# Optimization experiments

Measured on AMD Instinct MI355X. Metric: run time of the kernel, lower is better.

## Reference

```python
import jax, jax.numpy as jnp
import numpy as np

N_NODES = 200_000
N_EDGES = 6_400_000
N_GRAPHS = 512


def _sage_conv(x, edge_index, Wl, bl, Wr):
    """PyG SAGEConv (mean aggr): lin_l(mean_j x_j) + lin_r(x_i).
    lin_l has bias, lin_r does not. Messages flow src -> dst."""
    src, dst = edge_index[0], edge_index[1]
    n = x.shape[0]
    # gather neighbor features [E, F] and segment-mean into dst nodes
    msg_sum = jax.ops.segment_sum(x[src], dst, num_segments=n)
    deg = jax.ops.segment_sum(jnp.ones((src.shape[0],), x.dtype), dst, num_segments=n)
    mean = msg_sum / jnp.maximum(deg, 1.0)[:, None]  # zero in-degree -> 0
    return mean @ Wl.T + bl + x @ Wr.T


def setup_inputs() -> dict:
    key = jax.random.key(0)
    ks = jax.random.split(key, 9)
    x = jax.random.normal(ks[0], (N_NODES, 1), dtype=jnp.float32)
    edge_index = jax.random.randint(ks[1], (2, N_EDGES), 0, N_NODES, dtype=jnp.int64)
    batch = jnp.sort(jax.random.randint(ks[2], (N_NODES,), 0, N_GRAPHS, dtype=jnp.int64))
    W1l = jax.random.normal(ks[3], (16, 1), dtype=jnp.float32)
    b1 = jax.random.normal(ks[4], (16,), dtype=jnp.float32)
    W1r = jax.random.normal(ks[5], (16, 1), dtype=jnp.float32)
    W2l = jax.random.normal(ks[6], (1, 16), dtype=jnp.float32)
    b2 = jax.random.normal(ks[7], (1,), dtype=jnp.float32)
    W2r = jax.random.normal(ks[8], (1, 16), dtype=jnp.float32)
    return {"x": x, "edge_index": edge_index, "batch": batch, "batch_size": N_GRAPHS,
            "W1l": W1l, "b1": b1, "W1r": W1r, "W2l": W2l, "b2": b2, "W2r": W2r}


def reference(x, edge_index, batch, batch_size, W1l, b1, W1r, W2l, b2, W2r):
    h = _sage_conv(x, edge_index, W1l, b1, W1r)          # [N, 16]
    h = jax.nn.relu(h)
    h = _sage_conv(h, edge_index, W2l, b2, W2r)          # [N, 1]
    # global_add_pool: segment-sum node features by graph id
    out = jax.ops.segment_sum(h, batch, num_segments=batch_size)  # [B, 1]
    return out
```

## Files before the change

kernel.cpp:

```cpp
#include <hip/hip_runtime.h>


#define PP        16
#define BLK       1024
#define SCAP      1024u
#define SMASK     1023u
#define TILE      (BLK * 4)
#define CBIN      32
#define CNT_ONE   (1u << 25)
#define FX_BIAS   131072
#define SCALE     4096.0f
#define INV_SCALE (1.0f / 4096.0f)

__global__ __launch_bounds__(BLK) void partition_kernel(
    const int* __restrict__ ei, unsigned* __restrict__ pairs,
    unsigned* __restrict__ tails, int E, int bins, unsigned Mdiv, int cap) {
    extern __shared__ unsigned buf[];
    __shared__ unsigned cnt[PP], base[PP], fq[PP], gb[PP];
    const int tid = threadIdx.x;
    if (tid < PP) { cnt[tid] = 0; base[tid] = 0; }
    __syncthreads();

    int b0 = blockIdx.x * TILE;
    int e0 = b0 + tid * 4;
    int nv = E - e0; nv = nv < 0 ? 0 : (nv > 4 ? 4 : nv);
    int srcv[4], dstv[4];
    if (nv == 4 && ((E & 3) == 0)) {
        int4 s = *(const int4*)(ei + e0);
        int4 d = *(const int4*)(ei + E + e0);
        srcv[0] = s.x; srcv[1] = s.y; srcv[2] = s.z; srcv[3] = s.w;
        dstv[0] = d.x; dstv[1] = d.y; dstv[2] = d.z; dstv[3] = d.w;
    } else {
        for (int j = 0; j < nv; ++j) { srcv[j] = ei[e0 + j]; dstv[j] = ei[E + e0 + j]; }
    }
    unsigned w[4]; int part[4]; bool pend[4];
    for (int j = 0; j < 4; ++j) {
        pend[j] = (j < nv);
        if (pend[j]) {
            unsigned dst = (unsigned)dstv[j];
            unsigned pt = (unsigned)(((unsigned long long)dst * Mdiv) >> 32);
            int ld = (int)dst - (int)pt * bins;
            while (ld >= bins) { ld -= bins; ++pt; }
            while (ld < 0)     { ld += bins; --pt; }
            part[j] = (int)pt;
            w[j] = ((unsigned)srcv[j] << 14) | (unsigned)ld;
        }
    }
    for (int j = 0; j < 4; ++j) {
        if (pend[j]) {
            unsigned slot = atomicAdd(&cnt[part[j]], 1u);
            if (slot - base[part[j]] < SCAP) {
                buf[part[j] * SCAP + (slot & SMASK)] = w[j]; pend[j] = false;
            } else atomicSub(&cnt[part[j]], 1u);
        }
    }
    int npend = __syncthreads_count((int)(pend[0] | pend[1] | pend[2] | pend[3]));
    while (npend > 0) {
        if (tid < PP) {
            unsigned avail = cnt[tid] - base[tid];
            unsigned f = avail & ~511u;
            fq[tid] = f;
            if (f) gb[tid] = atomicAdd(&tails[tid], f);
        }
        __syncthreads();
        {
            int wv = tid >> 6, lane = tid & 63;
            unsigned f = fq[wv];
            if (f) {
                unsigned g0 = gb[wv], bs = base[wv];
                unsigned mx = (g0 + f <= (unsigned)cap) ? f : ((unsigned)cap > g0 ? (unsigned)cap - g0 : 0u);
                unsigned* dp = pairs + (size_t)wv * cap + g0;
                for (unsigned jj = lane; jj < mx; jj += 64)
                    dp[jj] = buf[wv * SCAP + ((bs + jj) & SMASK)];
            }
        }
        __syncthreads();
        if (tid < PP) base[tid] += fq[tid];
        __syncthreads();
        for (int j = 0; j < 4; ++j) {
            if (pend[j]) {
                unsigned slot = atomicAdd(&cnt[part[j]], 1u);
                if (slot - base[part[j]] < SCAP) {
                    buf[part[j] * SCAP + (slot & SMASK)] = w[j]; pend[j] = false;
                } else atomicSub(&cnt[part[j]], 1u);
            }
        }
        npend = __syncthreads_count((int)(pend[0] | pend[1] | pend[2] | pend[3]));
    }
    if (tid < PP) {
        unsigned avail = cnt[tid] - base[tid];
        fq[tid] = avail;
        if (avail) gb[tid] = atomicAdd(&tails[tid], avail);
    }
    __syncthreads();
    {
        int wv = tid >> 6, lane = tid & 63;
        unsigned f = fq[wv];
        if (f) {
            unsigned g0 = gb[wv], bs = base[wv];
            unsigned mx = (g0 + f <= (unsigned)cap) ? f : ((unsigned)cap > g0 ? (unsigned)cap - g0 : 0u);
            unsigned* dp = pairs + (size_t)wv * cap + g0;
            for (unsigned jj = lane; jj < mx; jj += 64)
                dp[jj] = buf[wv * SCAP + ((bs + jj) & SMASK)];
        }
    }
}

__global__ __launch_bounds__(BLK, 8) void bin1_kernel(
    const unsigned* __restrict__ pairs, const unsigned* __restrict__ tails,
    const float* __restrict__ x, unsigned* __restrict__ slab,
    int N, int bins, int cap) {
    extern __shared__ unsigned sb[];
    int p = blockIdx.x & (PP - 1);
    int c = blockIdx.x / PP;
    int len = (int)tails[p]; if (len > cap) len = cap;
    int st = (int)((long long)len * c / CBIN);
    int en = (int)((long long)len * (c + 1) / CBIN);
    for (int j = threadIdx.x; j < bins; j += BLK) sb[j] = 0;
    __syncthreads();
    const unsigned* bp = pairs + (size_t)p * cap;
    int st4 = (st + 3) & ~3;
    int en4 = en & ~3;
    int preEnd = st4 < en ? st4 : en;
    for (int e = st + (int)threadIdx.x; e < preEnd; e += BLK) {
        unsigned wv = bp[e];
        atomicAdd(&sb[wv & 16383u],
                  CNT_ONE + (unsigned)((int)rintf(x[wv >> 14] * SCALE) + FX_BIAS));
    }
    if (st4 < en4) {
        const uint4* bp4 = (const uint4*)(bp + st4);
        int n4 = (en4 - st4) >> 2;
        for (int e = threadIdx.x; e < n4; e += BLK) {
            uint4 wq = bp4[e];
            atomicAdd(&sb[wq.x & 16383u],
                      CNT_ONE + (unsigned)((int)rintf(x[wq.x >> 14] * SCALE) + FX_BIAS));
            atomicAdd(&sb[wq.y & 16383u],
                      CNT_ONE + (unsigned)((int)rintf(x[wq.y >> 14] * SCALE) + FX_BIAS));
            atomicAdd(&sb[wq.z & 16383u],
                      CNT_ONE + (unsigned)((int)rintf(x[wq.z >> 14] * SCALE) + FX_BIAS));
            atomicAdd(&sb[wq.w & 16383u],
                      CNT_ONE + (unsigned)((int)rintf(x[wq.w >> 14] * SCALE) + FX_BIAS));
        }
    }
    int tailSt = st4 > en4 ? st4 : en4;
    for (int e = tailSt + (int)threadIdx.x; e < en; e += BLK) {
        unsigned wv = bp[e];
        atomicAdd(&sb[wv & 16383u],
                  CNT_ONE + (unsigned)((int)rintf(x[wv >> 14] * SCALE) + FX_BIAS));
    }
    __syncthreads();
    unsigned* dst = slab + (size_t)c * N + (size_t)p * bins;
    int nb = N - p * bins; if (nb > bins) nb = bins;
    for (int j = threadIdx.x; j < nb; j += BLK) dst[j] = sb[j];
}

__global__ __launch_bounds__(BLK, 8) void bin2_kernel(
    const unsigned* __restrict__ pairs, const unsigned* __restrict__ tails,
    const float* __restrict__ pv, int* __restrict__ slab,
    int N, int bins, int cap) {
    extern __shared__ int sbi[];
    int p = blockIdx.x & (PP - 1);
    int c = blockIdx.x / PP;
    int len = (int)tails[p]; if (len > cap) len = cap;
    int st = (int)((long long)len * c / CBIN);
    int en = (int)((long long)len * (c + 1) / CBIN);
    for (int j = threadIdx.x; j < bins; j += BLK) sbi[j] = 0;
    __syncthreads();
    const unsigned* bp = pairs + (size_t)p * cap;
    int st4 = (st + 3) & ~3;
    int en4 = en & ~3;
    int preEnd = st4 < en ? st4 : en;
    for (int e = st + (int)threadIdx.x; e < preEnd; e += BLK) {
        unsigned wv = bp[e];
        atomicAdd(&sbi[wv & 16383u], (int)rintf(pv[wv >> 14] * SCALE));
    }
    if (st4 < en4) {
        const uint4* bp4 = (const uint4*)(bp + st4);
        int n4 = (en4 - st4) >> 2;
        for (int e = threadIdx.x; e < n4; e += BLK) {
            uint4 wq = bp4[e];
            atomicAdd(&sbi[wq.x & 16383u], (int)rintf(pv[wq.x >> 14] * SCALE));
            atomicAdd(&sbi[wq.y & 16383u], (int)rintf(pv[wq.y >> 14] * SCALE));
            atomicAdd(&sbi[wq.z & 16383u], (int)rintf(pv[wq.z >> 14] * SCALE));
            atomicAdd(&sbi[wq.w & 16383u], (int)rintf(pv[wq.w >> 14] * SCALE));
        }
    }
    int tailSt = st4 > en4 ? st4 : en4;
    for (int e = tailSt + (int)threadIdx.x; e < en; e += BLK) {
        unsigned wv = bp[e];
        atomicAdd(&sbi[wv & 16383u], (int)rintf(pv[wv >> 14] * SCALE));
    }
    __syncthreads();
    int* dst = slab + (size_t)c * N + (size_t)p * bins;
    int nb = N - p * bins; if (nb > bins) nb = bins;
    for (int j = threadIdx.x; j < nb; j += BLK) dst[j] = sbi[j];
}

__global__ void node_pass1_kernel(const float* __restrict__ x,
                                  const unsigned* __restrict__ slab,
                                  const float* __restrict__ W1l,
                                  const float* __restrict__ b1,
                                  const float* __restrict__ W1r,
                                  const float* __restrict__ W2l,
                                  const float* __restrict__ W2r,
                                  float* __restrict__ deg_out,
                                  float* __restrict__ pv,
                                  float* __restrict__ qv,
                                  int N) {
    __shared__ float s_w1l[16], s_b1[16], s_w1r[16], s_w2l[16], s_w2r[16];
    if (threadIdx.x < 16) {
        s_w1l[threadIdx.x] = W1l[threadIdx.x];
        s_b1[threadIdx.x]  = b1[threadIdx.x];
        s_w1r[threadIdx.x] = W1r[threadIdx.x];
        s_w2l[threadIdx.x] = W2l[threadIdx.x];
        s_w2r[threadIdx.x] = W2r[threadIdx.x];
    }
    __syncthreads();
    int n = blockIdx.x * blockDim.x + threadIdx.x;
    if (n >= N) return;

    unsigned cnt = 0, fx = 0;
#pragma unroll
    for (int c = 0; c < CBIN; ++c) {
        unsigned w = slab[(size_t)c * N + n];
        cnt += w >> 25;
        fx  += w & (CNT_ONE - 1);
    }
    float dg  = (float)cnt;
    float sum = (float)(int)(fx - cnt * (unsigned)FX_BIAS) * INV_SCALE;
    float m   = sum / fmaxf(dg, 1.0f);

    float xv = x[n];
    float pa = 0.0f, qa = 0.0f;
#pragma unroll
    for (int f = 0; f < 16; ++f) {
        float h = fmaf(m, s_w1l[f], fmaf(xv, s_w1r[f], s_b1[f]));
        h = fmaxf(h, 0.0f);
        pa = fmaf(h, s_w2l[f], pa);
        qa = fmaf(h, s_w2r[f], qa);
    }
    deg_out[n] = dg;
    pv[n] = pa;
    qv[n] = qa;
}

__global__ void node_pass2_kernel(const int* __restrict__ slab2,
                                  const float* __restrict__ deg,
                                  const float* __restrict__ qv,
                                  const float* __restrict__ b2,
                                  const int* __restrict__ batch,
                                  float* __restrict__ out,
                                  int N) {
    int i = blockIdx.x * blockDim.x + threadIdx.x;
    float b2v = b2[0];
    float val = 0.0f;
    int g;
    if (i < N) {
        int sacc = 0;
#pragma unroll
        for (int c = 0; c < CBIN; ++c) sacc += slab2[(size_t)c * N + i];
        float s2 = (float)sacc * INV_SCALE;
        val = s2 / fmaxf(deg[i], 1.0f) + b2v + qv[i];
        g = batch[i];
    } else {
        g = batch[N - 1];
    }
    int g0 = __shfl(g, 0);
    unsigned long long same = __ballot(g == g0);
    if (same == ~0ULL) {
        for (int off = 32; off > 0; off >>= 1) val += __shfl_down(val, off);
        if ((threadIdx.x & 63) == 0) atomicAdd(&out[g0], val);
    } else {
        atomicAdd(&out[g], val);
    }
}

extern "C" void kernel_launch(void* const* d_in, const int* in_sizes, int n_in,
                              void* d_out, int out_size, void* d_ws, size_t ws_size,
                              hipStream_t stream) {
    const float* x     = (const float*)d_in[0];
    const int*   ei    = (const int*)d_in[1];
    const int*   batch = (const int*)d_in[2];
    const float* W1l = (const float*)d_in[4];
    const float* b1  = (const float*)d_in[5];
    const float* W1r = (const float*)d_in[6];
    const float* W2l = (const float*)d_in[7];
    const float* b2  = (const float*)d_in[8];
    const float* W2r = (const float*)d_in[9];

    const int N = in_sizes[0];
    const int E = in_sizes[1] / 2;
    float* out = (float*)d_out;

    const int bins = (N + PP - 1) / PP;
    const unsigned Mdiv =
        (unsigned)(((1ULL << 32) + (unsigned)bins - 1) / (unsigned)bins);
    const int EperP = E / PP;
    int cap = ((EperP + EperP / 32 + 4096) + 1023) & ~1023;

    unsigned* pairs = (unsigned*)d_ws;
    unsigned* slab1 = pairs + (size_t)PP * cap;
    int*      slab2 = (int*)slab1;
    float* deg = (float*)(slab1 + (size_t)CBIN * N);
    float* pv  = deg + N;
    float* qv  = pv + N;
    unsigned* tails = (unsigned*)(qv + N);

    hipMemsetAsync(d_out, 0, (size_t)out_size * sizeof(float), stream);
    hipMemsetAsync(tails, 0, PP * sizeof(unsigned), stream);

    const int partShmem = PP * (int)SCAP * 4;
    const int binShmem  = bins * 4;
    hipFuncSetAttribute((const void*)partition_kernel,
                        hipFuncAttributeMaxDynamicSharedMemorySize, partShmem);
    hipFuncSetAttribute((const void*)bin1_kernel,
                        hipFuncAttributeMaxDynamicSharedMemorySize, binShmem);
    hipFuncSetAttribute((const void*)bin2_kernel,
                        hipFuncAttributeMaxDynamicSharedMemorySize, binShmem);

    int partBlocks = (E + TILE - 1) / TILE;
    const int NB = 256;
    int node_blocks = (N + NB - 1) / NB;

    partition_kernel<<<partBlocks, BLK, partShmem, stream>>>(ei, pairs, tails,
                                                             E, bins, Mdiv, cap);
    bin1_kernel<<<PP * CBIN, BLK, binShmem, stream>>>(pairs, tails, x, slab1,
                                                      N, bins, cap);
    node_pass1_kernel<<<node_blocks, NB, 0, stream>>>(x, slab1, W1l, b1, W1r,
                                                      W2l, W2r, deg, pv, qv, N);
    bin2_kernel<<<PP * CBIN, BLK, binShmem, stream>>>(pairs, tails, pv, slab2,
                                                      N, bins, cap);
    node_pass2_kernel<<<node_blocks, NB, 0, stream>>>(slab2, deg, qv, b2, batch,
                                                      out, N);
}
```

Measured before the change: 228.0 us.

## Replace partition-and-bin aggregation with direct global atomic scatter per edge

Removes the shared-memory partitioning pass and the LDS-binned slab reductions. Each edge pass now reads edge indices directly and performs global atomicAdd into per-node packed fixed-point accumulators, zeroed by a memset. This eliminates the intermediate pairs buffer write/read and the 32-way slab reduction, at the cost of 6.4M random global atomics per pass with no locality.

```diff
diff --git a/kernel.cpp b/kernel.cpp
--- a/kernel.cpp
+++ b/kernel.cpp
@@ -1,203 +1,62 @@
 #include <hip/hip_runtime.h>
 
 
-#define PP        16
-#define BLK       1024
-#define SCAP      1024u
-#define SMASK     1023u
-#define TILE      (BLK * 4)
-#define CBIN      32
 #define CNT_ONE   (1u << 25)
 #define FX_BIAS   131072
 #define SCALE     4096.0f
 #define INV_SCALE (1.0f / 4096.0f)
 
-__global__ __launch_bounds__(BLK) void partition_kernel(
-    const int* __restrict__ ei, unsigned* __restrict__ pairs,
-    unsigned* __restrict__ tails, int E, int bins, unsigned Mdiv, int cap) {
-    extern __shared__ unsigned buf[];
-    __shared__ unsigned cnt[PP], base[PP], fq[PP], gb[PP];
-    const int tid = threadIdx.x;
-    if (tid < PP) { cnt[tid] = 0; base[tid] = 0; }
-    __syncthreads();
-
-    int b0 = blockIdx.x * TILE;
-    int e0 = b0 + tid * 4;
-    int nv = E - e0; nv = nv < 0 ? 0 : (nv > 4 ? 4 : nv);
-    int srcv[4], dstv[4];
-    if (nv == 4 && ((E & 3) == 0)) {
+__global__ __launch_bounds__(256) void edge1_kernel(
+    const int* __restrict__ ei, const float* __restrict__ x,
+    unsigned* __restrict__ acc1, int E) {
+    int t = blockIdx.x * blockDim.x + threadIdx.x;
+    int e0 = t * 4;
+    if (e0 + 4 <= E) {
         int4 s = *(const int4*)(ei + e0);
         int4 d = *(const int4*)(ei + E + e0);
-        srcv[0] = s.x; srcv[1] = s.y; srcv[2] = s.z; srcv[3] = s.w;
-        dstv[0] = d.x; dstv[1] = d.y; dstv[2] = d.z; dstv[3] = d.w;
+        unsigned w0 = CNT_ONE + (unsigned)((int)rintf(x[s.x] * SCALE) + FX_BIAS);
+        unsigned w1 = CNT_ONE + (unsigned)((int)rintf(x[s.y] * SCALE) + FX_BIAS);
+        unsigned w2 = CNT_ONE + (unsigned)((int)rintf(x[s.z] * SCALE) + FX_BIAS);
+        unsigned w3 = CNT_ONE + (unsigned)((int)rintf(x[s.w] * SCALE) + FX_BIAS);
+        atomicAdd(&acc1[d.x], w0);
+        atomicAdd(&acc1[d.y], w1);
+        atomicAdd(&acc1[d.z], w2);
+        atomicAdd(&acc1[d.w], w3);
     } else {
-        for (int j = 0; j < nv; ++j) { srcv[j] = ei[e0 + j]; dstv[j] = ei[E + e0 + j]; }
-    }
-    unsigned w[4]; int part[4]; bool pend[4];
-    for (int j = 0; j < 4; ++j) {
-        pend[j] = (j < nv);
-        if (pend[j]) {
-            unsigned dst = (unsigned)dstv[j];
-            unsigned pt = (unsigned)(((unsigned long long)dst * Mdiv) >> 32);
-            int ld = (int)dst - (int)pt * bins;
-            while (ld >= bins) { ld -= bins; ++pt; }
-            while (ld < 0)     { ld += bins; --pt; }
-            part[j] = (int)pt;
-            w[j] = ((unsigned)srcv[j] << 14) | (unsigned)ld;
-        }
-    }
-    for (int j = 0; j < 4; ++j) {
-        if (pend[j]) {
-            unsigned slot = atomicAdd(&cnt[part[j]], 1u);
-            if (slot - base[part[j]] < SCAP) {
-                buf[part[j] * SCAP + (slot & SMASK)] = w[j]; pend[j] = false;
-            } else atomicSub(&cnt[part[j]], 1u);
-        }
-    }
-    int npend = __syncthreads_count((int)(pend[0] | pend[1] | pend[2] | pend[3]));
-    while (npend > 0) {
-        if (tid < PP) {
-            unsigned avail = cnt[tid] - base[tid];
-            unsigned f = avail & ~511u;
-            fq[tid] = f;
-            if (f) gb[tid] = atomicAdd(&tails[tid], f);
-        }
-        __syncthreads();
-        {
-            int wv = tid >> 6, lane = tid & 63;
-            unsigned f = fq[wv];
-            if (f) {
-                unsigned g0 = gb[wv], bs = base[wv];
-                unsigned mx = (g0 + f <= (unsigned)cap) ? f : ((unsigned)cap > g0 ? (unsigned)cap - g0 : 0u);
-                unsigned* dp = pairs + (size_t)wv * cap + g0;
-                for (unsigned jj = lane; jj < mx; jj += 64)
-                    dp[jj] = buf[wv * SCAP + ((bs + jj) & SMASK)];
-            }
-        }
-        __syncthreads();
-        if (tid < PP) base[tid] += fq[tid];
-        __syncthreads();
-        for (int j = 0; j < 4; ++j) {
-            if (pend[j]) {
-                unsigned slot = atomicAdd(&cnt[part[j]], 1u);
-                if (slot - base[part[j]] < SCAP) {
-                    buf[part[j] * SCAP + (slot & SMASK)] = w[j]; pend[j] = false;
-                } else atomicSub(&cnt[part[j]], 1u);
-            }
-        }
-        npend = __syncthreads_count((int)(pend[0] | pend[1] | pend[2] | pend[3]));
-    }
-    if (tid < PP) {
-        unsigned avail = cnt[tid] - base[tid];
-        fq[tid] = avail;
-        if (avail) gb[tid] = atomicAdd(&tails[tid], avail);
-    }
-    __syncthreads();
-    {
-        int wv = tid >> 6, lane = tid & 63;
-        unsigned f = fq[wv];
-        if (f) {
-            unsigned g0 = gb[wv], bs = base[wv];
-            unsigned mx = (g0 + f <= (unsigned)cap) ? f : ((unsigned)cap > g0 ? (unsigned)cap - g0 : 0u);
-            unsigned* dp = pairs + (size_t)wv * cap + g0;
-            for (unsigned jj = lane; jj < mx; jj += 64)
-                dp[jj] = buf[wv * SCAP + ((bs + jj) & SMASK)];
+        for (int e = e0; e < E; ++e) {
+            int s = ei[e], d = ei[E + e];
+            atomicAdd(&acc1[d],
+                      CNT_ONE + (unsigned)((int)rintf(x[s] * SCALE) + FX_BIAS));
         }
     }
 }
 
-__global__ __launch_bounds__(BLK, 8) void bin1_kernel(
-    const unsigned* __restrict__ pairs, const unsigned* __restrict__ tails,
-    const float* __restrict__ x, unsigned* __restrict__ slab,
-    int N, int bins, int cap) {
-    extern __shared__ unsigned sb[];
-    int p = blockIdx.x & (PP - 1);
-    int c = blockIdx.x / PP;
-    int len = (int)tails[p]; if (len > cap) len = cap;
-    int st = (int)((long long)len * c / CBIN);
-    int en = (int)((long long)len * (c + 1) / CBIN);
-    for (int j = threadIdx.x; j < bins; j += BLK) sb[j] = 0;
-    __syncthreads();
-    const unsigned* bp = pairs + (size_t)p * cap;
-    int st4 = (st + 3) & ~3;
-    int en4 = en & ~3;
-    int preEnd = st4 < en ? st4 : en;
-    for (int e = st + (int)threadIdx.x; e < preEnd; e += BLK) {
-        unsigned wv = bp[e];
-        atomicAdd(&sb[wv & 16383u],
-                  CNT_ONE + (unsigned)((int)rintf(x[wv >> 14] * SCALE) + FX_BIAS));
-    }
-    if (st4 < en4) {
-        const uint4* bp4 = (const uint4*)(bp + st4);
-        int n4 = (en4 - st4) >> 2;
-        for (int e = threadIdx.x; e < n4; e += BLK) {
-            uint4 wq = bp4[e];
-            atomicAdd(&sb[wq.x & 16383u],
-                      CNT_ONE + (unsigned)((int)rintf(x[wq.x >> 14] * SCALE) + FX_BIAS));
-            atomicAdd(&sb[wq.y & 16383u],
-                      CNT_ONE + (unsigned)((int)rintf(x[wq.y >> 14] * SCALE) + FX_BIAS));
-            atomicAdd(&sb[wq.z & 16383u],
-                      CNT_ONE + (unsigned)((int)rintf(x[wq.z >> 14] * SCALE) + FX_BIAS));
-            atomicAdd(&sb[wq.w & 16383u],
-                      CNT_ONE + (unsigned)((int)rintf(x[wq.w >> 14] * SCALE) + FX_BIAS));
+__global__ __launch_bounds__(256) void edge2_kernel(
+    const int* __restrict__ ei, const float* __restrict__ pv,
+    int* __restrict__ acc2, int E) {
+    int t = blockIdx.x * blockDim.x + threadIdx.x;
+    int e0 = t * 4;
+    if (e0 + 4 <= E) {
+        int4 s = *(const int4*)(ei + e0);
+        int4 d = *(const int4*)(ei + E + e0);
+        int v0 = (int)rintf(pv[s.x] * SCALE);
+        int v1 = (int)rintf(pv[s.y] * SCALE);
+        int v2 = (int)rintf(pv[s.z] * SCALE);
+        int v3 = (int)rintf(pv[s.w] * SCALE);
+        atomicAdd(&acc2[d.x], v0);
+        atomicAdd(&acc2[d.y], v1);
+        atomicAdd(&acc2[d.z], v2);
+        atomicAdd(&acc2[d.w], v3);
+    } else {
+        for (int e = e0; e < E; ++e) {
+            int s = ei[e], d = ei[E + e];
+            atomicAdd(&acc2[d], (int)rintf(pv[s] * SCALE));
         }
     }
-    int tailSt = st4 > en4 ? st4 : en4;
-    for (int e = tailSt + (int)threadIdx.x; e < en; e += BLK) {
-        unsigned wv = bp[e];
-        atomicAdd(&sb[wv & 16383u],
-                  CNT_ONE + (unsigned)((int)rintf(x[wv >> 14] * SCALE) + FX_BIAS));
-    }
-    __syncthreads();
-    unsigned* dst = slab + (size_t)c * N + (size_t)p * bins;
-    int nb = N - p * bins; if (nb > bins) nb = bins;
-    for (int j = threadIdx.x; j < nb; j += BLK) dst[j] = sb[j];
-}
-
-__global__ __launch_bounds__(BLK, 8) void bin2_kernel(
-    const unsigned* __restrict__ pairs, const unsigned* __restrict__ tails,
-    const float* __restrict__ pv, int* __restrict__ slab,
-    int N, int bins, int cap) {
-    extern __shared__ int sbi[];
-    int p = blockIdx.x & (PP - 1);
-    int c = blockIdx.x / PP;
-    int len = (int)tails[p]; if (len > cap) len = cap;
-    int st = (int)((long long)len * c / CBIN);
-    int en = (int)((long long)len * (c + 1) / CBIN);
-    for (int j = threadIdx.x; j < bins; j += BLK) sbi[j] = 0;
-    __syncthreads();
-    const unsigned* bp = pairs + (size_t)p * cap;
-    int st4 = (st + 3) & ~3;
-    int en4 = en & ~3;
-    int preEnd = st4 < en ? st4 : en;
-    for (int e = st + (int)threadIdx.x; e < preEnd; e += BLK) {
-        unsigned wv = bp[e];
-        atomicAdd(&sbi[wv & 16383u], (int)rintf(pv[wv >> 14] * SCALE));
-    }
-    if (st4 < en4) {
-        const uint4* bp4 = (const uint4*)(bp + st4);
-        int n4 = (en4 - st4) >> 2;
-        for (int e = threadIdx.x; e < n4; e += BLK) {
-            uint4 wq = bp4[e];
-            atomicAdd(&sbi[wq.x & 16383u], (int)rintf(pv[wq.x >> 14] * SCALE));
-            atomicAdd(&sbi[wq.y & 16383u], (int)rintf(pv[wq.y >> 14] * SCALE));
-            atomicAdd(&sbi[wq.z & 16383u], (int)rintf(pv[wq.z >> 14] * SCALE));
-            atomicAdd(&sbi[wq.w & 16383u], (int)rintf(pv[wq.w >> 14] * SCALE));
-        }
-    }
-    int tailSt = st4 > en4 ? st4 : en4;
-    for (int e = tailSt + (int)threadIdx.x; e < en; e += BLK) {
-        unsigned wv = bp[e];
-        atomicAdd(&sbi[wv & 16383u], (int)rintf(pv[wv >> 14] * SCALE));
-    }
-    __syncthreads();
-    int* dst = slab + (size_t)c * N + (size_t)p * bins;
-    int nb = N - p * bins; if (nb > bins) nb = bins;
-    for (int j = threadIdx.x; j < nb; j += BLK) dst[j] = sbi[j];
 }
 
 __global__ void node_pass1_kernel(const float* __restrict__ x,
-                                  const unsigned* __restrict__ slab,
+                                  const unsigned* __restrict__ acc1,
                                   const float* __restrict__ W1l,
                                   const float* __restrict__ b1,
                                   const float* __restrict__ W1r,
@@ -219,13 +78,9 @@
     int n = blockIdx.x * blockDim.x + threadIdx.x;
     if (n >= N) return;
 
-    unsigned cnt = 0, fx = 0;
-#pragma unroll
-    for (int c = 0; c < CBIN; ++c) {
-        unsigned w = slab[(size_t)c * N + n];
-        cnt += w >> 25;
-        fx  += w & (CNT_ONE - 1);
-    }
+    unsigned w = acc1[n];
+    unsigned cnt = w >> 25;
+    unsigned fx  = w & (CNT_ONE - 1);
     float dg  = (float)cnt;
     float sum = (float)(int)(fx - cnt * (unsigned)FX_BIAS) * INV_SCALE;
     float m   = sum / fmaxf(dg, 1.0f);
@@ -244,7 +99,7 @@
     qv[n] = qa;
 }
 
-__global__ void node_pass2_kernel(const int* __restrict__ slab2,
+__global__ void node_pass2_kernel(const int* __restrict__ acc2,
                                   const float* __restrict__ deg,
                                   const float* __restrict__ qv,
                                   const float* __restrict__ b2,
@@ -256,10 +111,7 @@
     float val = 0.0f;
     int g;
     if (i < N) {
-        int sacc = 0;
-#pragma unroll
-        for (int c = 0; c < CBIN; ++c) sacc += slab2[(size_t)c * N + i];
-        float s2 = (float)sacc * INV_SCALE;
+        float s2 = (float)acc2[i] * INV_SCALE;
         val = s2 / fmaxf(deg[i], 1.0f) + b2v + qv[i];
         g = batch[i];
     } else {
@@ -292,44 +144,24 @@
     const int E = in_sizes[1] / 2;
     float* out = (float*)d_out;
 
-    const int bins = (N + PP - 1) / PP;
-    const unsigned Mdiv =
-        (unsigned)(((1ULL << 32) + (unsigned)bins - 1) / (unsigned)bins);
-    const int EperP = E / PP;
-    int cap = ((EperP + EperP / 32 + 4096) + 1023) & ~1023;
-
-    unsigned* pairs = (unsigned*)d_ws;
-    unsigned* slab1 = pairs + (size_t)PP * cap;
-    int*      slab2 = (int*)slab1;
-    float* deg = (float*)(slab1 + (size_t)CBIN * N);
+    unsigned* acc1 = (unsigned*)d_ws;
+    int*      acc2 = (int*)(acc1 + N);
+    float* deg = (float*)(acc2 + N);
     float* pv  = deg + N;
     float* qv  = pv + N;
-    unsigned* tails = (unsigned*)(qv + N);
 
     hipMemsetAsync(d_out, 0, (size_t)out_size * sizeof(float), stream);
-    hipMemsetAsync(tails, 0, PP * sizeof(unsigned), stream);
+    hipMemsetAsync(acc1, 0, (size_t)(2 * N) * 4, stream);
 
-    const int partShmem = PP * (int)SCAP * 4;
-    const int binShmem  = bins * 4;
-    hipFuncSetAttribute((const void*)partition_kernel,
-                        hipFuncAttributeMaxDynamicSharedMemorySize, partShmem);
-    hipFuncSetAttribute((const void*)bin1_kernel,
-                        hipFuncAttributeMaxDynamicSharedMemorySize, binShmem);
-    hipFuncSetAttribute((const void*)bin2_kernel,
-                        hipFuncAttributeMaxDynamicSharedMemorySize, binShmem);
-
-    int partBlocks = (E + TILE - 1) / TILE;
+    const int EB = 256;
+    int edge_blocks = (E / 4 + EB - 1) / EB;
     const int NB = 256;
     int node_blocks = (N + NB - 1) / NB;
 
-    partition_kernel<<<partBlocks, BLK, partShmem, stream>>>(ei, pairs, tails,
-                                                             E, bins, Mdiv, cap);
-    bin1_kernel<<<PP * CBIN, BLK, binShmem, stream>>>(pairs, tails, x, slab1,
-                                                      N, bins, cap);
-    node_pass1_kernel<<<node_blocks, NB, 0, stream>>>(x, slab1, W1l, b1, W1r,
+    edge1_kernel<<<edge_blocks, EB, 0, stream>>>(ei, x, acc1, E);
+    node_pass1_kernel<<<node_blocks, NB, 0, stream>>>(x, acc1, W1l, b1, W1r,
                                                       W2l, W2r, deg, pv, qv, N);
-    bin2_kernel<<<PP * CBIN, BLK, binShmem, stream>>>(pairs, tails, pv, slab2,
-                                                      N, bins, cap);
-    node_pass2_kernel<<<node_blocks, NB, 0, stream>>>(slab2, deg, qv, b2, batch,
+    edge2_kernel<<<edge_blocks, EB, 0, stream>>>(ei, pv, acc2, E);
+    node_pass2_kernel<<<node_blocks, NB, 0, stream>>>(acc2, deg, qv, b2, batch,
                                                       out, N);
 }
```

After: 622.0 us. 2.73x slower.

## Use power-of-two bins, prequantize gathers, and atomically merge partial histograms

Applied to the files above, without the earlier changes.

Partitions destinations with a 16384-node shift/mask instead of a magic-number division, which gives 13 partitions for this N instead of 16. Node features are quantized once up front, in a new prequant kernel and in node_pass1, so the per-edge loops only gather integers. Each bin block now atomically adds its nonzero LDS histogram entries into one global accumulator instead of writing a full per-chunk slab that the node kernels then reduce over 32 rows. This cuts slab traffic and reduction work, in exchange for global atomics, an extra launch, a larger memset, and a changed chunk count of 39.

```diff
diff --git a/kernel.cpp b/kernel.cpp
--- a/kernel.cpp
+++ b/kernel.cpp
@@ -1,24 +1,33 @@
 #include <hip/hip_runtime.h>
 
 
-#define PP        16
 #define BLK       1024
 #define SCAP      1024u
 #define SMASK     1023u
 #define TILE      (BLK * 4)
-#define CBIN      32
+#define BSH       14
+#define BINS      16384
+#define BMSK      16383u
+#define CBIN      39
 #define CNT_ONE   (1u << 25)
 #define FX_BIAS   131072
 #define SCALE     4096.0f
 #define INV_SCALE (1.0f / 4096.0f)
 
+__global__ __launch_bounds__(256) void prequant_kernel(
+    const float* __restrict__ x, unsigned* __restrict__ xq1, int N) {
+    int n = blockIdx.x * blockDim.x + threadIdx.x;
+    if (n < N)
+        xq1[n] = CNT_ONE + (unsigned)((int)rintf(x[n] * SCALE) + FX_BIAS);
+}
+
 __global__ __launch_bounds__(BLK) void partition_kernel(
     const int* __restrict__ ei, unsigned* __restrict__ pairs,
-    unsigned* __restrict__ tails, int E, int bins, unsigned Mdiv, int cap) {
+    unsigned* __restrict__ tails, int E, int cap, int pp) {
     extern __shared__ unsigned buf[];
-    __shared__ unsigned cnt[PP], base[PP], fq[PP], gb[PP];
+    __shared__ unsigned cnt[16], base[16], fq[16], gb[16];
     const int tid = threadIdx.x;
-    if (tid < PP) { cnt[tid] = 0; base[tid] = 0; }
+    if (tid < pp) { cnt[tid] = 0; base[tid] = 0; }
     __syncthreads();
 
     int b0 = blockIdx.x * TILE;
@@ -38,12 +47,8 @@
         pend[j] = (j < nv);
         if (pend[j]) {
             unsigned dst = (unsigned)dstv[j];
-            unsigned pt = (unsigned)(((unsigned long long)dst * Mdiv) >> 32);
-            int ld = (int)dst - (int)pt * bins;
-            while (ld >= bins) { ld -= bins; ++pt; }
-            while (ld < 0)     { ld += bins; --pt; }
-            part[j] = (int)pt;
-            w[j] = ((unsigned)srcv[j] << 14) | (unsigned)ld;
+            part[j] = (int)(dst >> BSH);
+            w[j] = ((unsigned)srcv[j] << BSH) | (dst & BMSK);
         }
     }
     for (int j = 0; j < 4; ++j) {
@@ -56,7 +61,7 @@
     }
     int npend = __syncthreads_count((int)(pend[0] | pend[1] | pend[2] | pend[3]));
     while (npend > 0) {
-        if (tid < PP) {
+        if (tid < pp) {
             unsigned avail = cnt[tid] - base[tid];
             unsigned f = avail & ~511u;
             fq[tid] = f;
@@ -65,6 +70,39 @@
         __syncthreads();
         {
             int wv = tid >> 6, lane = tid & 63;
+            if (wv < pp) {
+                unsigned f = fq[wv];
+                if (f) {
+                    unsigned g0 = gb[wv], bs = base[wv];
+                    unsigned mx = (g0 + f <= (unsigned)cap) ? f : ((unsigned)cap > g0 ? (unsigned)cap - g0 : 0u);
+                    unsigned* dp = pairs + (size_t)wv * cap + g0;
+                    for (unsigned jj = lane; jj < mx; jj += 64)
+                        dp[jj] = buf[wv * SCAP + ((bs + jj) & SMASK)];
+                }
+            }
+        }
+        __syncthreads();
+        if (tid < pp) base[tid] += fq[tid];
+        __syncthreads();
+        for (int j = 0; j < 4; ++j) {
+            if (pend[j]) {
+                unsigned slot = atomicAdd(&cnt[part[j]], 1u);
+                if (slot - base[part[j]] < SCAP) {
+                    buf[part[j] * SCAP + (slot & SMASK)] = w[j]; pend[j] = false;
+                } else atomicSub(&cnt[part[j]], 1u);
+            }
+        }
+        npend = __syncthreads_count((int)(pend[0] | pend[1] | pend[2] | pend[3]));
+    }
+    if (tid < pp) {
+        unsigned avail = cnt[tid] - base[tid];
+        fq[tid] = avail;
+        if (avail) gb[tid] = atomicAdd(&tails[tid], avail);
+    }
+    __syncthreads();
+    {
+        int wv = tid >> 6, lane = tid & 63;
+        if (wv < pp) {
             unsigned f = fq[wv];
             if (f) {
                 unsigned g0 = gb[wv], bs = base[wv];
@@ -74,137 +112,118 @@
                     dp[jj] = buf[wv * SCAP + ((bs + jj) & SMASK)];
             }
         }
-        __syncthreads();
-        if (tid < PP) base[tid] += fq[tid];
-        __syncthreads();
-        for (int j = 0; j < 4; ++j) {
-            if (pend[j]) {
-                unsigned slot = atomicAdd(&cnt[part[j]], 1u);
-                if (slot - base[part[j]] < SCAP) {
-                    buf[part[j] * SCAP + (slot & SMASK)] = w[j]; pend[j] = false;
-                } else atomicSub(&cnt[part[j]], 1u);
-            }
-        }
-        npend = __syncthreads_count((int)(pend[0] | pend[1] | pend[2] | pend[3]));
-    }
-    if (tid < PP) {
-        unsigned avail = cnt[tid] - base[tid];
-        fq[tid] = avail;
-        if (avail) gb[tid] = atomicAdd(&tails[tid], avail);
-    }
-    __syncthreads();
-    {
-        int wv = tid >> 6, lane = tid & 63;
-        unsigned f = fq[wv];
-        if (f) {
-            unsigned g0 = gb[wv], bs = base[wv];
-            unsigned mx = (g0 + f <= (unsigned)cap) ? f : ((unsigned)cap > g0 ? (unsigned)cap - g0 : 0u);
-            unsigned* dp = pairs + (size_t)wv * cap + g0;
-            for (unsigned jj = lane; jj < mx; jj += 64)
-                dp[jj] = buf[wv * SCAP + ((bs + jj) & SMASK)];
-        }
     }
 }
 
 __global__ __launch_bounds__(BLK, 8) void bin1_kernel(
     const unsigned* __restrict__ pairs, const unsigned* __restrict__ tails,
-    const float* __restrict__ x, unsigned* __restrict__ slab,
-    int N, int bins, int cap) {
-    extern __shared__ unsigned sb[];
-    int p = blockIdx.x & (PP - 1);
-    int c = blockIdx.x / PP;
+    const unsigned* __restrict__ xq1, unsigned* __restrict__ acc1,
+    int N, int cap) {
+    extern __shared__ unsigned sbn[];
+    const int tid = threadIdx.x;
+    const int p = blockIdx.x;
+    const int c = blockIdx.y;
+    for (int j = tid; j < BINS; j += BLK) sbn[j] = 0;
+    __syncthreads();
     int len = (int)tails[p]; if (len > cap) len = cap;
     int st = (int)((long long)len * c / CBIN);
     int en = (int)((long long)len * (c + 1) / CBIN);
-    for (int j = threadIdx.x; j < bins; j += BLK) sb[j] = 0;
-    __syncthreads();
     const unsigned* bp = pairs + (size_t)p * cap;
     int st4 = (st + 3) & ~3;
     int en4 = en & ~3;
     int preEnd = st4 < en ? st4 : en;
-    for (int e = st + (int)threadIdx.x; e < preEnd; e += BLK) {
+    for (int e = st + tid; e < preEnd; e += BLK) {
         unsigned wv = bp[e];
-        atomicAdd(&sb[wv & 16383u],
-                  CNT_ONE + (unsigned)((int)rintf(x[wv >> 14] * SCALE) + FX_BIAS));
+        atomicAdd(&sbn[wv & BMSK], xq1[wv >> BSH]);
     }
     if (st4 < en4) {
         const uint4* bp4 = (const uint4*)(bp + st4);
         int n4 = (en4 - st4) >> 2;
-        for (int e = threadIdx.x; e < n4; e += BLK) {
+        for (int e = tid; e < n4; e += BLK) {
             uint4 wq = bp4[e];
-            atomicAdd(&sb[wq.x & 16383u],
-                      CNT_ONE + (unsigned)((int)rintf(x[wq.x >> 14] * SCALE) + FX_BIAS));
-            atomicAdd(&sb[wq.y & 16383u],
-                      CNT_ONE + (unsigned)((int)rintf(x[wq.y >> 14] * SCALE) + FX_BIAS));
-            atomicAdd(&sb[wq.z & 16383u],
-                      CNT_ONE + (unsigned)((int)rintf(x[wq.z >> 14] * SCALE) + FX_BIAS));
-            atomicAdd(&sb[wq.w & 16383u],
-                      CNT_ONE + (unsigned)((int)rintf(x[wq.w >> 14] * SCALE) + FX_BIAS));
+            unsigned p0 = xq1[wq.x >> BSH];
+            unsigned p1 = xq1[wq.y >> BSH];
+            unsigned p2 = xq1[wq.z >> BSH];
+            unsigned p3 = xq1[wq.w >> BSH];
+            atomicAdd(&sbn[wq.x & BMSK], p0);
+            atomicAdd(&sbn[wq.y & BMSK], p1);
+            atomicAdd(&sbn[wq.z & BMSK], p2);
+            atomicAdd(&sbn[wq.w & BMSK], p3);
         }
     }
     int tailSt = st4 > en4 ? st4 : en4;
-    for (int e = tailSt + (int)threadIdx.x; e < en; e += BLK) {
+    for (int e = tailSt + tid; e < en; e += BLK) {
         unsigned wv = bp[e];
-        atomicAdd(&sb[wv & 16383u],
-                  CNT_ONE + (unsigned)((int)rintf(x[wv >> 14] * SCALE) + FX_BIAS));
-    }
-    __syncthreads();
-    unsigned* dst = slab + (size_t)c * N + (size_t)p * bins;
-    int nb = N - p * bins; if (nb > bins) nb = bins;
-    for (int j = threadIdx.x; j < nb; j += BLK) dst[j] = sb[j];
+        atomicAdd(&sbn[wv & BMSK], xq1[wv >> BSH]);
+    }
+    __syncthreads();
+    unsigned* dst = acc1 + ((size_t)p << BSH);
+    int nb = N - (p << BSH); if (nb > BINS) nb = BINS;
+    for (int j = tid; j < nb; j += BLK) {
+        unsigned v = sbn[j];
+        if (v) atomicAdd(&dst[j], v);
+    }
 }
 
 __global__ __launch_bounds__(BLK, 8) void bin2_kernel(
     const unsigned* __restrict__ pairs, const unsigned* __restrict__ tails,
-    const float* __restrict__ pv, int* __restrict__ slab,
-    int N, int bins, int cap) {
+    const int* __restrict__ pvq, int* __restrict__ acc2,
+    int N, int cap) {
     extern __shared__ int sbi[];
-    int p = blockIdx.x & (PP - 1);
-    int c = blockIdx.x / PP;
+    const int tid = threadIdx.x;
+    const int p = blockIdx.x;
+    const int c = blockIdx.y;
+    for (int j = tid; j < BINS; j += BLK) sbi[j] = 0;
+    __syncthreads();
     int len = (int)tails[p]; if (len > cap) len = cap;
     int st = (int)((long long)len * c / CBIN);
     int en = (int)((long long)len * (c + 1) / CBIN);
-    for (int j = threadIdx.x; j < bins; j += BLK) sbi[j] = 0;
-    __syncthreads();
     const unsigned* bp = pairs + (size_t)p * cap;
     int st4 = (st + 3) & ~3;
     int en4 = en & ~3;
     int preEnd = st4 < en ? st4 : en;
-    for (int e = st + (int)threadIdx.x; e < preEnd; e += BLK) {
+    for (int e = st + tid; e < preEnd; e += BLK) {
         unsigned wv = bp[e];
-        atomicAdd(&sbi[wv & 16383u], (int)rintf(pv[wv >> 14] * SCALE));
+        atomicAdd(&sbi[wv & BMSK], pvq[wv >> BSH]);
     }
     if (st4 < en4) {
         const uint4* bp4 = (const uint4*)(bp + st4);
         int n4 = (en4 - st4) >> 2;
-        for (int e = threadIdx.x; e < n4; e += BLK) {
+        for (int e = tid; e < n4; e += BLK) {
             uint4 wq = bp4[e];
-            atomicAdd(&sbi[wq.x & 16383u], (int)rintf(pv[wq.x >> 14] * SCALE));
-            atomicAdd(&sbi[wq.y & 16383u], (int)rintf(pv[wq.y >> 14] * SCALE));
-            atomicAdd(&sbi[wq.z & 16383u], (int)rintf(pv[wq.z >> 14] * SCALE));
-            atomicAdd(&sbi[wq.w & 16383u], (int)rintf(pv[wq.w >> 14] * SCALE));
+            int p0 = pvq[wq.x >> BSH];
+            int p1 = pvq[wq.y >> BSH];
+            int p2 = pvq[wq.z >> BSH];
+            int p3 = pvq[wq.w >> BSH];
+            atomicAdd(&sbi[wq.x & BMSK], p0);
+            atomicAdd(&sbi[wq.y & BMSK], p1);
+            atomicAdd(&sbi[wq.z & BMSK], p2);
+            atomicAdd(&sbi[wq.w & BMSK], p3);
         }
     }
     int tailSt = st4 > en4 ? st4 : en4;
-    for (int e = tailSt + (int)threadIdx.x; e < en; e += BLK) {
+    for (int e = tailSt + tid; e < en; e += BLK) {
         unsigned wv = bp[e];
-        atomicAdd(&sbi[wv & 16383u], (int)rintf(pv[wv >> 14] * SCALE));
-    }
-    __syncthreads();
-    int* dst = slab + (size_t)c * N + (size_t)p * bins;
-    int nb = N - p * bins; if (nb > bins) nb = bins;
-    for (int j = threadIdx.x; j < nb; j += BLK) dst[j] = sbi[j];
+        atomicAdd(&sbi[wv & BMSK], pvq[wv >> BSH]);
+    }
+    __syncthreads();
+    int* dst = acc2 + ((size_t)p << BSH);
+    int nb = N - (p << BSH); if (nb > BINS) nb = BINS;
+    for (int j = tid; j < nb; j += BLK) {
+        int v = sbi[j];
+        if (v) atomicAdd(&dst[j], v);
+    }
 }
 
 __global__ void node_pass1_kernel(const float* __restrict__ x,
-                                  const unsigned* __restrict__ slab,
+                                  const unsigned* __restrict__ acc1,
                                   const float* __restrict__ W1l,
                                   const float* __restrict__ b1,
                                   const float* __restrict__ W1r,
                                   const float* __restrict__ W2l,
                                   const float* __restrict__ W2r,
                                   float* __restrict__ deg_out,
-                                  float* __restrict__ pv,
+                                  int* __restrict__ pvq,
                                   float* __restrict__ qv,
                                   int N) {
     __shared__ float s_w1l[16], s_b1[16], s_w1r[16], s_w2l[16], s_w2r[16];
@@ -219,13 +238,9 @@
     int n = blockIdx.x * blockDim.x + threadIdx.x;
     if (n >= N) return;
 
-    unsigned cnt = 0, fx = 0;
-#pragma unroll
-    for (int c = 0; c < CBIN; ++c) {
-        unsigned w = slab[(size_t)c * N + n];
-        cnt += w >> 25;
-        fx  += w & (CNT_ONE - 1);
-    }
+    unsigned w = acc1[n];
+    unsigned cnt = w >> 25;
+    unsigned fx  = w & (CNT_ONE - 1);
     float dg  = (float)cnt;
     float sum = (float)(int)(fx - cnt * (unsigned)FX_BIAS) * INV_SCALE;
     float m   = sum / fmaxf(dg, 1.0f);
@@ -240,11 +255,11 @@
         qa = fmaf(h, s_w2r[f], qa);
     }
     deg_out[n] = dg;
-    pv[n] = pa;
+    pvq[n] = (int)rintf(pa * SCALE);
     qv[n] = qa;
 }
 
-__global__ void node_pass2_kernel(const int* __restrict__ slab2,
+__global__ void node_pass2_kernel(const int* __restrict__ acc2,
                                   const float* __restrict__ deg,
                                   const float* __restrict__ qv,
                                   const float* __restrict__ b2,
@@ -256,10 +271,7 @@
     float val = 0.0f;
     int g;
     if (i < N) {
-        int sacc = 0;
-#pragma unroll
-        for (int c = 0; c < CBIN; ++c) sacc += slab2[(size_t)c * N + i];
-        float s2 = (float)sacc * INV_SCALE;
+        float s2 = (float)acc2[i] * INV_SCALE;
         val = s2 / fmaxf(deg[i], 1.0f) + b2v + qv[i];
         g = batch[i];
     } else {
@@ -292,25 +304,24 @@
     const int E = in_sizes[1] / 2;
     float* out = (float*)d_out;
 
-    const int bins = (N + PP - 1) / PP;
-    const unsigned Mdiv =
-        (unsigned)(((1ULL << 32) + (unsigned)bins - 1) / (unsigned)bins);
-    const int EperP = E / PP;
-    int cap = ((EperP + EperP / 32 + 4096) + 1023) & ~1023;
+    const int pp = (N + BINS - 1) >> BSH;
+    long long expMax = ((long long)E * BINS + N - 1) / N;
+    int cap = (int)((expMax + 32768 + 1023) & ~1023LL);
 
     unsigned* pairs = (unsigned*)d_ws;
-    unsigned* slab1 = pairs + (size_t)PP * cap;
-    int*      slab2 = (int*)slab1;
-    float* deg = (float*)(slab1 + (size_t)CBIN * N);
-    float* pv  = deg + N;
-    float* qv  = pv + N;
-    unsigned* tails = (unsigned*)(qv + N);
+    unsigned* acc1  = pairs + (size_t)pp * cap;
+    int*      acc2  = (int*)(acc1 + N);
+    unsigned* tails = (unsigned*)(acc2 + N);
+    unsigned* xq1   = tails + 16;
+    float* deg = (float*)(xq1 + N);
+    int*   pvq = (int*)(deg + N);
+    float* qv  = (float*)(pvq + N);
 
     hipMemsetAsync(d_out, 0, (size_t)out_size * sizeof(float), stream);
-    hipMemsetAsync(tails, 0, PP * sizeof(unsigned), stream);
-
-    const int partShmem = PP * (int)SCAP * 4;
-    const int binShmem  = bins * 4;
+    hipMemsetAsync(acc1, 0, (size_t)(2 * N + 16) * 4, stream);
+
+    const int partShmem = pp * (int)SCAP * 4;
+    const int binShmem  = BINS * 4;
     hipFuncSetAttribute((const void*)partition_kernel,
                         hipFuncAttributeMaxDynamicSharedMemorySize, partShmem);
     hipFuncSetAttribute((const void*)bin1_kernel,
@@ -322,14 +333,15 @@
     const int NB = 256;
     int node_blocks = (N + NB - 1) / NB;
 
+    prequant_kernel<<<node_blocks, NB, 0, stream>>>(x, xq1, N);
     partition_kernel<<<partBlocks, BLK, partShmem, stream>>>(ei, pairs, tails,
-                                                             E, bins, Mdiv, cap);
-    bin1_kernel<<<PP * CBIN, BLK, binShmem, stream>>>(pairs, tails, x, slab1,
-                                                      N, bins, cap);
-    node_pass1_kernel<<<node_blocks, NB, 0, stream>>>(x, slab1, W1l, b1, W1r,
-                                                      W2l, W2r, deg, pv, qv, N);
-    bin2_kernel<<<PP * CBIN, BLK, binShmem, stream>>>(pairs, tails, pv, slab2,
-                                                      N, bins, cap);
-    node_pass2_kernel<<<node_blocks, NB, 0, stream>>>(slab2, deg, qv, b2, batch,
+                                                             E, cap, pp);
+    bin1_kernel<<<dim3(pp, CBIN), BLK, binShmem, stream>>>(pairs, tails, xq1,
+                                                           acc1, N, cap);
+    node_pass1_kernel<<<node_blocks, NB, 0, stream>>>(x, acc1, W1l, b1, W1r,
+                                                      W2l, W2r, deg, pvq, qv, N);
+    bin2_kernel<<<dim3(pp, CBIN), BLK, binShmem, stream>>>(pairs, tails, pvq,
+                                                           acc2, N, cap);
+    node_pass2_kernel<<<node_blocks, NB, 0, stream>>>(acc2, deg, qv, b2, batch,
                                                       out, N);
 }
```

Result: slower. 243.6 us (+6.9%).
